# Kernel optimization log

Measured on AMD Instinct MI355X. Metric: run time of the kernel, lower is better.

## Reference

```python
import jax, jax.numpy as jnp
import numpy as np
from functools import partial

STRIDES = (8, 16, 32)
SCORE_THRESH = 0.3
NMS_THRESH = 0.5
TOPK = 500          # fixed pre-NMS candidate count (jit-friendly substitute for boolean masking)
CLASS_OFFSET = 1e4  # offset boxes per class so cross-class IoU == 0 -> per-class NMS


def _decode(cls, reg, obj, stride):
    # cls [B,C,H,W], reg [B,4,H,W], obj [B,1,H,W]
    B, C, H, W = cls.shape
    yv, xv = jnp.meshgrid(jnp.arange(H, dtype=cls.dtype), jnp.arange(W, dtype=cls.dtype), indexing='ij')
    scores = jax.nn.sigmoid(obj) * jax.nn.sigmoid(cls)          # [B,C,H,W]
    dx, dy, dw, dh = reg[:, 0], reg[:, 1], reg[:, 2], reg[:, 3]
    cx = (xv + jax.nn.sigmoid(dx)) * stride
    cy = (yv + jax.nn.sigmoid(dy)) * stride
    w = jnp.exp(dw) * stride
    h = jnp.exp(dh) * stride
    boxes = jnp.stack([cx - w / 2, cy - h / 2, cx + w / 2, cy + h / 2], axis=-1)  # [B,H,W,4]
    return boxes.reshape(B, H * W, 4), scores.reshape(B, C, H * W).transpose(0, 2, 1)


def _pairwise_iou(boxes):
    # boxes [B,K,4] xyxy -> iou [B,K,K]
    area = (boxes[..., 2] - boxes[..., 0]) * (boxes[..., 3] - boxes[..., 1])
    x1 = jnp.maximum(boxes[:, :, None, 0], boxes[:, None, :, 0])
    y1 = jnp.maximum(boxes[:, :, None, 1], boxes[:, None, :, 1])
    x2 = jnp.minimum(boxes[:, :, None, 2], boxes[:, None, :, 2])
    y2 = jnp.minimum(boxes[:, :, None, 3], boxes[:, None, :, 3])
    inter = jnp.clip(x2 - x1, 0) * jnp.clip(y2 - y1, 0)
    union = area[:, :, None] + area[:, None, :] - inter
    return inter / (union + 1e-7)


def _greedy_nms(iou, valid):
    # iou [B,K,K], valid [B,K] -> keep [B,K]; greedy over score-sorted order (axis 1)
    B, K = valid.shape
    def step(supp, i):
        keep_i = valid[:, i] & ~supp[:, i]                    # [B]
        supp = supp | (keep_i[:, None] & (iou[:, i, :] >= NMS_THRESH))
        return supp, keep_i
    _, keep_t = jax.lax.scan(step, jnp.zeros((B, K), dtype=bool), jnp.arange(K))
    return keep_t.T  # [B,K]


def _predict(levels):
    boxes_l, scores_l = [], []
    for (c, r, o), s in zip(levels, STRIDES):
        b, sc = _decode(c, r, o, s)
        boxes_l.append(b)
        scores_l.append(sc)
    boxes = jnp.concatenate(boxes_l, axis=1)     # [B,N,4]
    scores = jnp.concatenate(scores_l, axis=1)   # [B,N,C]
    max_scores = scores.max(axis=-1)             # [B,N]
    labels = jnp.argmax(scores, axis=-1)         # [B,N]
    masked = jnp.where(max_scores > SCORE_THRESH, max_scores, -1.0)
    top_scores, idx = jax.lax.top_k(masked, TOPK)                         # sorted desc
    top_boxes = jnp.take_along_axis(boxes, idx[..., None], axis=1)        # [B,K,4]
    top_labels = jnp.take_along_axis(labels, idx, axis=1)                 # [B,K]
    valid = top_scores > SCORE_THRESH
    boxes_off = top_boxes + (top_labels.astype(top_boxes.dtype) * CLASS_OFFSET)[..., None]
    keep = _greedy_nms(_pairwise_iou(boxes_off), valid)                   # [B,K]
    out_boxes = jnp.where(keep[..., None], top_boxes, 0.0)
    out_scores = jnp.where(keep, top_scores, 0.0)
    return out_boxes, out_scores, top_labels, keep


def setup_inputs() -> dict:
    key = jax.random.key(0)
    ks = jax.random.split(key, 9)
    B, C = 64, 2
    shapes = {
        'cls_p3': (B, C, 160, 160), 'reg_p3': (B, 4, 160, 160), 'obj_p3': (B, 1, 160, 160),
        'cls_p4': (B, C, 80, 80),   'reg_p4': (B, 4, 80, 80),   'obj_p4': (B, 1, 80, 80),
        'cls_p5': (B, C, 40, 40),   'reg_p5': (B, 4, 40, 40),   'obj_p5': (B, 1, 40, 40),
    }
    return {name: jax.random.normal(k, shp, dtype=jnp.float32)
            for k, (name, shp) in zip(ks, shapes.items())}


def reference(cls_p3, reg_p3, obj_p3, cls_p4, reg_p4, obj_p4, cls_p5, reg_p5, obj_p5):
    levels = [(cls_p3, reg_p3, obj_p3), (cls_p4, reg_p4, obj_p4), (cls_p5, reg_p5, obj_p5)]
    return _predict(levels)
```

## Files before the change

### kernel.cpp

```cpp
#include <hip/hip_runtime.h>
#include <hip/hip_bf16.h>
#include <stdint.h>

#define NB 64
#define NA 33600
#define NK 500
#define HW3 25600
#define HW4 6400
#define HW5 1600
#define OFF4 25600
#define OFF5 32000
#define NBIN 2048
#define NA4 8400
#define LCAP 1024
#define MROWS 512

typedef unsigned int u32;
typedef unsigned long long u64;

__device__ __forceinline__ float sigf(float x) { return 1.0f / (1.0f + expf(-x)); }

__device__ __forceinline__ u32 f2key(float f) {
  u32 u = __float_as_uint(f);
  return (u & 0x80000000u) ? ~u : (u | 0x80000000u);
}
__device__ __forceinline__ float key2f(u32 k) {
  u32 u = (k & 0x80000000u) ? (k ^ 0x80000000u) : ~k;
  return __uint_as_float(u);
}
__device__ __forceinline__ int bin_of(float s) {
  int b = (int)(s * 2048.0f);
  return b > 2047 ? 2047 : b;
}
__device__ __forceinline__ u32 mkkey(float o, float c0, float c1) {
  float so = sigf(o);
  float s = fmaxf(so * sigf(c0), so * sigf(c1));
  float masked = (s > 0.3f) ? s : -1.0f;
  return f2key(masked);
}
__device__ __forceinline__ u64 uniform64(u64 v) {
  u32 lo = (u32)__builtin_amdgcn_readfirstlane((int)(u32)v);
  u32 hi = (u32)__builtin_amdgcn_readfirstlane((int)(u32)(v >> 32));
  return ((u64)hi << 32) | lo;
}

__global__ __launch_bounds__(256) void k_score(
    const float* __restrict__ cls3, const float* __restrict__ obj3,
    const float* __restrict__ cls4, const float* __restrict__ obj4,
    const float* __restrict__ cls5, const float* __restrict__ obj5,
    uint4* __restrict__ keys4)
{
  int b = blockIdx.y;
  int i4 = blockIdx.x * 256 + threadIdx.x;
  if (i4 >= NA4) return;
  const float* cls; const float* obj; int p4, HW;
  if (i4 < 6400)      { cls = cls3; obj = obj3; p4 = i4;        HW = HW3; }
  else if (i4 < 8000) { cls = cls4; obj = obj4; p4 = i4 - 6400; HW = HW4; }
  else                { cls = cls5; obj = obj5; p4 = i4 - 8000; HW = HW5; }
  float4 o  = reinterpret_cast<const float4*>(obj + (size_t)b * HW)[p4];
  float4 c0 = reinterpret_cast<const float4*>(cls + (size_t)(b * 2) * HW)[p4];
  float4 c1 = reinterpret_cast<const float4*>(cls + (size_t)(b * 2 + 1) * HW)[p4];
  uint4 kv;
  kv.x = mkkey(o.x, c0.x, c1.x);
  kv.y = mkkey(o.y, c0.y, c1.y);
  kv.z = mkkey(o.z, c0.z, c1.z);
  kv.w = mkkey(o.w, c0.w, c1.w);
  keys4[(size_t)b * NA4 + i4] = kv;
}

__global__ __launch_bounds__(1024) void k_topk(
    const u32* __restrict__ keys,
    const float* __restrict__ cls3, const float* __restrict__ obj3, const float* __restrict__ reg3,
    const float* __restrict__ cls4, const float* __restrict__ obj4, const float* __restrict__ reg4,
    const float* __restrict__ cls5, const float* __restrict__ obj5, const float* __restrict__ reg5,
    float* __restrict__ top_score,
    float4* __restrict__ boxes, float4* __restrict__ boxesoff,
    float* __restrict__ out_labels)
{
  int b = blockIdx.x, tid = threadIdx.x;
  __shared__ u32 hist[NBIN];
  __shared__ u32 part[256];
  __shared__ u64 cand[LCAP];
  __shared__ int idx_lds[NK];
  __shared__ float score_lds[NK];
  __shared__ u32 lcnt;
  __shared__ int sh_p;
  __shared__ u32 sh_R;
  __shared__ int sh_digit;
  __shared__ u32 sh_cnt;

  for (int i = tid; i < NBIN; i += 1024) hist[i] = 0;
  if (tid == 0) lcnt = 0;
  __syncthreads();

  const u32* kb = keys + (size_t)b * NA;
  const uint4* kb4 = reinterpret_cast<const uint4*>(kb);

  uint4 kreg[9];
#pragma unroll
  for (int k = 0; k < 9; ++k) {
    int i4 = tid + k * 1024;
    kreg[k] = (i4 < NA4) ? kb4[i4] : make_uint4(0u, 0u, 0u, 0u);
  }

#pragma unroll
  for (int k = 0; k < 9; ++k) {
    u32 ks[4] = {kreg[k].x, kreg[k].y, kreg[k].z, kreg[k].w};
#pragma unroll
    for (int c = 0; c < 4; ++c) {
      float s = key2f(ks[c]);
      if (s > 0.3f) atomicAdd(&hist[bin_of(s)], 1u);
    }
  }
  __syncthreads();
  if (tid < 256) {
    u32 s8 = 0;
#pragma unroll
    for (int k = 0; k < 8; ++k) s8 += hist[tid * 8 + k];
    part[tid] = s8;
  }
  __syncthreads();
  for (int off = 1; off < 256; off <<= 1) {
    u32 add = 0;
    if (tid < 256 && tid + off < 256) add = part[tid + off];
    __syncthreads();
    if (tid < 256) part[tid] += add;
    __syncthreads();
  }
  if (tid == 0 && part[0] < NK) sh_p = -1;
  if (tid < 256) {
    u32 S = part[tid];
    u32 Snext = (tid == 255) ? 0u : part[tid + 1];
    if (S >= NK && Snext < NK) {
      u32 run = Snext;
      int p = tid * 8;
      for (int k = 7; k >= 0; --k) {
        run += hist[tid * 8 + k];
        if (run >= NK) { p = tid * 8 + k; break; }
      }
      sh_p = p;
    }
  }
  __syncthreads();
  int p = sh_p;
  bool fail = (p < 0);
  if (!fail) {
#pragma unroll
    for (int k = 0; k < 9; ++k) {
      int i4 = tid + k * 1024;
      u32 ks[4] = {kreg[k].x, kreg[k].y, kreg[k].z, kreg[k].w};
#pragma unroll
      for (int c = 0; c < 4; ++c) {
        float s = key2f(ks[c]);
        if (s > 0.3f && bin_of(s) >= p) {
          u32 slot = atomicAdd(&lcnt, 1u);
          if (slot < LCAP) cand[slot] = ((u64)ks[c] << 16) | (u32)(0xFFFF - (i4 * 4 + c));
        }
      }
    }
    __syncthreads();
    fail = (lcnt > LCAP);
  }

  if (!fail) {
    for (int i = lcnt + tid; i < LCAP; i += 1024) cand[i] = 0;
    for (int k = 2; k <= LCAP; k <<= 1) {
      for (int j = k >> 1; j > 0; j >>= 1) {
        __syncthreads();
        if (tid < LCAP / 2) {
          int i = ((tid & ~(j - 1)) << 1) | (tid & (j - 1));
          int ixj = i | j;
          u64 a = cand[i], c2 = cand[ixj];
          bool dir = ((i & k) == 0);
          if ((a < c2) == dir) { cand[i] = c2; cand[ixj] = a; }
        }
      }
    }
    __syncthreads();
    if (tid < NK) {
      u64 kk = cand[tid];
      idx_lds[tid] = 0xFFFF - (int)(kk & 0xFFFFull);
      score_lds[tid] = key2f((u32)(kk >> 16));
    }
  } else {
    u64 prefix = 0, prefmask = 0;
    u32 R = NK;
    for (int pass = 0; pass < 6; ++pass) {
      int shift = 40 - 8 * pass;
      if (tid < 256) part[tid] = 0;
      __syncthreads();
      for (int i = tid; i < NA; i += 1024) {
        u64 k48 = ((u64)kb[i] << 16) | (u32)(0xFFFF - i);
        if ((k48 & prefmask) == prefix)
          atomicAdd(&part[(u32)(k48 >> shift) & 255u], 1u);
      }
      __syncthreads();
      if (tid < 256) hist[tid] = part[tid];
      __syncthreads();
      for (int off = 1; off < 256; off <<= 1) {
        u32 add = 0;
        if (tid < 256 && tid + off < 256) add = hist[tid + off];
        __syncthreads();
        if (tid < 256) hist[tid] += add;
        __syncthreads();
      }
      if (tid < 256) {
        u32 s = hist[tid];
        u32 snext = (tid == 255) ? 0u : hist[tid + 1];
        if (s >= R && snext < R) { sh_digit = tid; sh_R = R - snext; }
      }
      __syncthreads();
      prefix |= ((u64)sh_digit) << shift;
      R = sh_R;
      prefmask |= 0xFFull << shift;
      __syncthreads();
    }
    if (tid == 0) sh_cnt = 0;
    if (tid < NK) { idx_lds[tid] = 0; score_lds[tid] = -1.0f; }
    __syncthreads();
    for (int i = tid; i < NA; i += 1024) {
      u64 k48 = ((u64)kb[i] << 16) | (u32)(0xFFFF - i);
      if (k48 >= prefix) {
        u32 slot = atomicAdd(&sh_cnt, 1u);
        if (slot < 512) cand[slot] = k48;
      }
    }
    __syncthreads();
    int n = (sh_cnt < (u32)NK) ? (int)sh_cnt : NK;
    for (int t = tid; t < n; t += 1024) {
      u64 k = cand[t];
      int rank = 0;
      for (int j = 0; j < n; ++j) rank += (cand[j] > k) ? 1 : 0;
      if (rank < NK) {
        idx_lds[rank] = 0xFFFF - (int)(k & 0xFFFFull);
        score_lds[rank] = key2f((u32)(k >> 16));
      }
    }
  }
  __syncthreads();

  if (tid < NK) {
    int a = idx_lds[tid];
    const float *cls, *obj, *reg; int pos, HW, x, y; float stride;
    if (a < OFF4) {
      cls = cls3; obj = obj3; reg = reg3; pos = a; HW = HW3; stride = 8.0f;
      y = pos / 160; x = pos - y * 160;
    } else if (a < OFF5) {
      cls = cls4; obj = obj4; reg = reg4; pos = a - OFF4; HW = HW4; stride = 16.0f;
      y = pos / 80; x = pos - y * 80;
    } else {
      cls = cls5; obj = obj5; reg = reg5; pos = a - OFF5; HW = HW5; stride = 32.0f;
      y = pos / 40; x = pos - y * 40;
    }
    float dx = reg[(b * 4 + 0) * HW + pos];
    float dy = reg[(b * 4 + 1) * HW + pos];
    float dw = reg[(b * 4 + 2) * HW + pos];
    float dh = reg[(b * 4 + 3) * HW + pos];
    float cx = ((float)x + sigf(dx)) * stride;
    float cy = ((float)y + sigf(dy)) * stride;
    float w = expf(dw) * stride;
    float h = expf(dh) * stride;
    float x1 = cx - w * 0.5f, y1 = cy - h * 0.5f;
    float x2 = cx + w * 0.5f, y2 = cy + h * 0.5f;
    float so = sigf(obj[b * HW + pos]);
    float s0 = so * sigf(cls[(b * 2) * HW + pos]);
    float s1 = so * sigf(cls[(b * 2 + 1) * HW + pos]);
    int label = (s1 > s0) ? 1 : 0;
    float off = (float)label * 10000.0f;
    int t = b * NK + tid;
    boxes[t]    = make_float4(x1, y1, x2, y2);
    boxesoff[t] = make_float4(x1 + off, y1 + off, x2 + off, y2 + off);
    out_labels[t] = (float)label;
    top_score[t] = score_lds[tid];
  }
}

__global__ __launch_bounds__(256) void k_iou(
    const float4* __restrict__ boxesoff, u64* __restrict__ mask)
{
  int t = blockIdx.x * 256 + threadIdx.x;
  if (t >= NB * NK * 8) return;
  int w = t & 7;
  int bi = t >> 3;
  int b = bi / NK;
  int i = bi - b * NK;
  float4 A = boxesoff[bi];
  float areaA = (A.z - A.x) * (A.w - A.y);
  const float4* base = boxesoff + b * NK;
  int j0 = w * 64;
  int jmax = (NK - j0 < 64) ? (NK - j0) : 64;
  u64 bits = 0;
  for (int jj = 0; jj < jmax; ++jj) {
    float4 Bx = base[j0 + jj];
    float areaB = (Bx.z - Bx.x) * (Bx.w - Bx.y);
    float ix1 = fmaxf(A.x, Bx.x);
    float iy1 = fmaxf(A.y, Bx.y);
    float ix2 = fminf(A.z, Bx.z);
    float iy2 = fminf(A.w, Bx.w);
    float iw = fmaxf(ix2 - ix1, 0.0f);
    float ih = fmaxf(iy2 - iy1, 0.0f);
    float inter = iw * ih;
    float uni = areaA + areaB - inter;
    float iou = inter / (uni + 1e-7f);
    bits |= ((u64)(iou >= 0.5f)) << jj;
  }
  mask[(size_t)b * (MROWS * 8) + (size_t)i * 8 + w] = bits;
}

__global__ __launch_bounds__(64) void k_nms(
    const u64* __restrict__ mask, const float* __restrict__ top_score,
    const float4* __restrict__ boxes,
    float* __restrict__ out_boxes, float* __restrict__ out_scores,
    float* __restrict__ out_keep)
{
  int b = blockIdx.x;
  int lane = threadIdx.x;
  const u64* mb = mask + (size_t)b * (MROWS * 8);

  u64 validw[8];
#pragma unroll
  for (int c = 0; c < 8; ++c) {
    int r = c * 64 + lane;
    float s = (r < NK) ? top_score[b * NK + r] : -1.0f;
    validw[c] = __ballot(s > 0.3f);
  }

  u64 supp[8] = {0, 0, 0, 0, 0, 0, 0, 0};
  u64 keepw[8];
  u64 row[2][8];

  {
    const u64* rp = mb + (size_t)lane * 8;
#pragma unroll
    for (int w = 0; w < 8; ++w) row[0][w] = rp[w];
  }

#pragma unroll
  for (int c = 0; c < 8; ++c) {
    const int cur = c & 1, nxt = cur ^ 1;
    if (c < 7) {
      const u64* rp = mb + (size_t)((c + 1) * 64 + lane) * 8;
#pragma unroll
      for (int w = 0; w < 8; ++w)
        if (w >= c + 1) row[nxt][w] = rp[w];
    }
    u32 rlo = (u32)row[cur][c];
    u32 rhi = (u32)(row[cur][c] >> 32);
    u64 sw = supp[c], vw = validw[c], km = 0;
#pragma unroll
    for (int i = 0; i < 64; ++i) {
      u64 wi = ((u64)(u32)__builtin_amdgcn_readlane(rhi, i) << 32) |
               (u64)(u32)__builtin_amdgcn_readlane(rlo, i);
      u64 bit = 1ull << i;
      if ((vw & bit) && !(sw & bit)) { sw |= wi; km |= bit; }
    }
    keepw[c] = km;
    u64 sel = ((km >> lane) & 1ull) ? ~0ull : 0ull;
#pragma unroll
    for (int w = c + 1; w < 8; ++w) {
      u64 v = row[cur][w] & sel;
#pragma unroll
      for (int off = 1; off < 64; off <<= 1)
        v |= (u64)__shfl_xor((unsigned long long)v, off, 64);
      supp[w] |= uniform64(v);
    }
  }

#pragma unroll
  for (int c = 0; c < 8; ++c) {
    int r = c * 64 + lane;
    if (r < NK) {
      int kp = (int)((keepw[c] >> lane) & 1ull);
      float4 bx = boxes[b * NK + r];
      float s = top_score[b * NK + r];
      float4 ob;
      ob.x = kp ? bx.x : 0.0f;
      ob.y = kp ? bx.y : 0.0f;
      ob.z = kp ? bx.z : 0.0f;
      ob.w = kp ? bx.w : 0.0f;
      reinterpret_cast<float4*>(out_boxes)[b * NK + r] = ob;
      out_scores[b * NK + r] = kp ? s : 0.0f;
      out_keep[b * NK + r]   = kp ? 1.0f : 0.0f;
    }
  }
}

extern "C" void kernel_launch(void* const* d_in, const int* in_sizes, int n_in,
                              void* d_out, int out_size, void* d_ws, size_t ws_size,
                              hipStream_t stream) {
  const float* cls3 = (const float*)d_in[0];
  const float* reg3 = (const float*)d_in[1];
  const float* obj3 = (const float*)d_in[2];
  const float* cls4 = (const float*)d_in[3];
  const float* reg4 = (const float*)d_in[4];
  const float* obj4 = (const float*)d_in[5];
  const float* cls5 = (const float*)d_in[6];
  const float* reg5 = (const float*)d_in[7];
  const float* obj5 = (const float*)d_in[8];

  char* ws = (char*)d_ws;
  u32*    keys      = (u32*)   (ws + 0);
  float*  top_score = (float*) (ws + 8601600);
  float4* boxes     = (float4*)(ws + 8729600);
  float4* boxesoff  = (float4*)(ws + 9241600);
  u64*    mask      = (u64*)   (ws + 9753600);

  float* out        = (float*)d_out;
  float* out_boxes  = out;
  float* out_scores = out + 128000;
  float* out_labels = out + 160000;
  float* out_keep   = out + 192000;

  dim3 gscore((NA4 + 255) / 256, NB);
  k_score<<<gscore, 256, 0, stream>>>(cls3, obj3, cls4, obj4, cls5, obj5, (uint4*)keys);
  k_topk<<<NB, 1024, 0, stream>>>(keys,
      cls3, obj3, reg3, cls4, obj4, reg4, cls5, obj5, reg5,
      top_score, boxes, boxesoff, out_labels);
  k_iou<<<(NB * NK * 8 + 255) / 256, 256, 0, stream>>>(boxesoff, mask);
  k_nms<<<NB, 64, 0, stream>>>(mask, top_score, boxes, out_boxes, out_scores, out_keep);
}
```

Measured before the change: 95.10 us.

## Fuse score/key computation into top-k kernel and reuse keys from registers

```diff
diff --git a/kernel.cpp b/kernel.cpp
--- a/kernel.cpp
+++ b/kernel.cpp
@@ -44,32 +44,7 @@
   return ((u64)hi << 32) | lo;
 }
 
-__global__ __launch_bounds__(256) void k_score(
-    const float* __restrict__ cls3, const float* __restrict__ obj3,
-    const float* __restrict__ cls4, const float* __restrict__ obj4,
-    const float* __restrict__ cls5, const float* __restrict__ obj5,
-    uint4* __restrict__ keys4)
-{
-  int b = blockIdx.y;
-  int i4 = blockIdx.x * 256 + threadIdx.x;
-  if (i4 >= NA4) return;
-  const float* cls; const float* obj; int p4, HW;
-  if (i4 < 6400)      { cls = cls3; obj = obj3; p4 = i4;        HW = HW3; }
-  else if (i4 < 8000) { cls = cls4; obj = obj4; p4 = i4 - 6400; HW = HW4; }
-  else                { cls = cls5; obj = obj5; p4 = i4 - 8000; HW = HW5; }
-  float4 o  = reinterpret_cast<const float4*>(obj + (size_t)b * HW)[p4];
-  float4 c0 = reinterpret_cast<const float4*>(cls + (size_t)(b * 2) * HW)[p4];
-  float4 c1 = reinterpret_cast<const float4*>(cls + (size_t)(b * 2 + 1) * HW)[p4];
-  uint4 kv;
-  kv.x = mkkey(o.x, c0.x, c1.x);
-  kv.y = mkkey(o.y, c0.y, c1.y);
-  kv.z = mkkey(o.z, c0.z, c1.z);
-  kv.w = mkkey(o.w, c0.w, c1.w);
-  keys4[(size_t)b * NA4 + i4] = kv;
-}
-
 __global__ __launch_bounds__(1024) void k_topk(
-    const u32* __restrict__ keys,
     const float* __restrict__ cls3, const float* __restrict__ obj3, const float* __restrict__ reg3,
     const float* __restrict__ cls4, const float* __restrict__ obj4, const float* __restrict__ reg4,
     const float* __restrict__ cls5, const float* __restrict__ obj5, const float* __restrict__ reg5,
@@ -93,14 +68,25 @@
   if (tid == 0) lcnt = 0;
   __syncthreads();
 
-  const u32* kb = keys + (size_t)b * NA;
-  const uint4* kb4 = reinterpret_cast<const uint4*>(kb);
-
   uint4 kreg[9];
 #pragma unroll
   for (int k = 0; k < 9; ++k) {
     int i4 = tid + k * 1024;
-    kreg[k] = (i4 < NA4) ? kb4[i4] : make_uint4(0u, 0u, 0u, 0u);
+    uint4 kv = make_uint4(0u, 0u, 0u, 0u);
+    if (i4 < NA4) {
+      const float* cls; const float* obj; int p4, HW;
+      if (i4 < 6400)      { cls = cls3; obj = obj3; p4 = i4;        HW = HW3; }
+      else if (i4 < 8000) { cls = cls4; obj = obj4; p4 = i4 - 6400; HW = HW4; }
+      else                { cls = cls5; obj = obj5; p4 = i4 - 8000; HW = HW5; }
+      float4 o  = reinterpret_cast<const float4*>(obj + (size_t)b * HW)[p4];
+      float4 c0 = reinterpret_cast<const float4*>(cls + (size_t)(b * 2) * HW)[p4];
+      float4 c1 = reinterpret_cast<const float4*>(cls + (size_t)(b * 2 + 1) * HW)[p4];
+      kv.x = mkkey(o.x, c0.x, c1.x);
+      kv.y = mkkey(o.y, c0.y, c1.y);
+      kv.z = mkkey(o.z, c0.z, c1.z);
+      kv.w = mkkey(o.w, c0.w, c1.w);
+    }
+    kreg[k] = kv;
   }
 
 #pragma unroll
@@ -189,10 +175,18 @@
       int shift = 40 - 8 * pass;
       if (tid < 256) part[tid] = 0;
       __syncthreads();
-      for (int i = tid; i < NA; i += 1024) {
-        u64 k48 = ((u64)kb[i] << 16) | (u32)(0xFFFF - i);
-        if ((k48 & prefmask) == prefix)
-          atomicAdd(&part[(u32)(k48 >> shift) & 255u], 1u);
+#pragma unroll
+      for (int k = 0; k < 9; ++k) {
+        int i4 = tid + k * 1024;
+        if (i4 < NA4) {
+          u32 ks[4] = {kreg[k].x, kreg[k].y, kreg[k].z, kreg[k].w};
+#pragma unroll
+          for (int c = 0; c < 4; ++c) {
+            u64 k48 = ((u64)ks[c] << 16) | (u32)(0xFFFF - (i4 * 4 + c));
+            if ((k48 & prefmask) == prefix)
+              atomicAdd(&part[(u32)(k48 >> shift) & 255u], 1u);
+          }
+        }
       }
       __syncthreads();
       if (tid < 256) hist[tid] = part[tid];
@@ -218,11 +212,19 @@
     if (tid == 0) sh_cnt = 0;
     if (tid < NK) { idx_lds[tid] = 0; score_lds[tid] = -1.0f; }
     __syncthreads();
-    for (int i = tid; i < NA; i += 1024) {
-      u64 k48 = ((u64)kb[i] << 16) | (u32)(0xFFFF - i);
-      if (k48 >= prefix) {
-        u32 slot = atomicAdd(&sh_cnt, 1u);
-        if (slot < 512) cand[slot] = k48;
+#pragma unroll
+    for (int k = 0; k < 9; ++k) {
+      int i4 = tid + k * 1024;
+      if (i4 < NA4) {
+        u32 ks[4] = {kreg[k].x, kreg[k].y, kreg[k].z, kreg[k].w};
+#pragma unroll
+        for (int c = 0; c < 4; ++c) {
+          u64 k48 = ((u64)ks[c] << 16) | (u32)(0xFFFF - (i4 * 4 + c));
+          if (k48 >= prefix) {
+            u32 slot = atomicAdd(&sh_cnt, 1u);
+            if (slot < 512) cand[slot] = k48;
+          }
+        }
       }
     }
     __syncthreads();
@@ -347,7 +349,7 @@
     u32 rlo = (u32)row[cur][c];
     u32 rhi = (u32)(row[cur][c] >> 32);
     u64 sw = supp[c], vw = validw[c], km = 0;
-#pragma unroll
+#pragma unroll 1
     for (int i = 0; i < 64; ++i) {
       u64 wi = ((u64)(u32)__builtin_amdgcn_readlane(rhi, i) << 32) |
                (u64)(u32)__builtin_amdgcn_readlane(rlo, i);
@@ -399,11 +401,10 @@
   const float* obj5 = (const float*)d_in[8];
 
   char* ws = (char*)d_ws;
-  u32*    keys      = (u32*)   (ws + 0);
-  float*  top_score = (float*) (ws + 8601600);
-  float4* boxes     = (float4*)(ws + 8729600);
-  float4* boxesoff  = (float4*)(ws + 9241600);
-  u64*    mask      = (u64*)   (ws + 9753600);
+  float*  top_score = (float*) (ws + 0);
+  float4* boxes     = (float4*)(ws + 128000);
+  float4* boxesoff  = (float4*)(ws + 640000);
+  u64*    mask      = (u64*)   (ws + 1152000);
 
   float* out        = (float*)d_out;
   float* out_boxes  = out;
@@ -411,9 +412,7 @@
   float* out_labels = out + 160000;
   float* out_keep   = out + 192000;
 
-  dim3 gscore((NA4 + 255) / 256, NB);
-  k_score<<<gscore, 256, 0, stream>>>(cls3, obj3, cls4, obj4, cls5, obj5, (uint4*)keys);
-  k_topk<<<NB, 1024, 0, stream>>>(keys,
+  k_topk<<<NB, 1024, 0, stream>>>(
       cls3, obj3, reg3, cls4, obj4, reg4, cls5, obj5, reg5,
       top_score, boxes, boxesoff, out_labels);
   k_iou<<<(NB * NK * 8 + 255) / 256, 256, 0, stream>>>(boxesoff, mask);
```

New measurement: 117.3 us. +23.3%, slower.

## Split top-k into grid-wide histogram, pivot, and collect kernels; defer NMS OR-reductions

Applied to the files above, without the earlier changes.

```diff
diff --git a/kernel.cpp b/kernel.cpp
--- a/kernel.cpp
+++ b/kernel.cpp
@@ -10,11 +10,13 @@
 #define HW5 1600
 #define OFF4 25600
 #define OFF5 32000
-#define NBIN 2048
 #define NA4 8400
+#define NSEG 33
+#define NBIN 256
 #define LCAP 1024
 #define MROWS 512
 
+typedef unsigned short u16;
 typedef unsigned int u32;
 typedef unsigned long long u64;
 
@@ -29,8 +31,8 @@
   return __uint_as_float(u);
 }
 __device__ __forceinline__ int bin_of(float s) {
-  int b = (int)(s * 2048.0f);
-  return b > 2047 ? 2047 : b;
+  int b = (int)(s * 256.0f);
+  return b > 255 ? 255 : b;
 }
 __device__ __forceinline__ u32 mkkey(float o, float c0, float c1) {
   float so = sigf(o);
@@ -48,28 +50,110 @@
     const float* __restrict__ cls3, const float* __restrict__ obj3,
     const float* __restrict__ cls4, const float* __restrict__ obj4,
     const float* __restrict__ cls5, const float* __restrict__ obj5,
-    uint4* __restrict__ keys4)
-{
-  int b = blockIdx.y;
-  int i4 = blockIdx.x * 256 + threadIdx.x;
-  if (i4 >= NA4) return;
-  const float* cls; const float* obj; int p4, HW;
-  if (i4 < 6400)      { cls = cls3; obj = obj3; p4 = i4;        HW = HW3; }
-  else if (i4 < 8000) { cls = cls4; obj = obj4; p4 = i4 - 6400; HW = HW4; }
-  else                { cls = cls5; obj = obj5; p4 = i4 - 8000; HW = HW5; }
-  float4 o  = reinterpret_cast<const float4*>(obj + (size_t)b * HW)[p4];
-  float4 c0 = reinterpret_cast<const float4*>(cls + (size_t)(b * 2) * HW)[p4];
-  float4 c1 = reinterpret_cast<const float4*>(cls + (size_t)(b * 2 + 1) * HW)[p4];
-  uint4 kv;
-  kv.x = mkkey(o.x, c0.x, c1.x);
-  kv.y = mkkey(o.y, c0.y, c1.y);
-  kv.z = mkkey(o.z, c0.z, c1.z);
-  kv.w = mkkey(o.w, c0.w, c1.w);
-  keys4[(size_t)b * NA4 + i4] = kv;
-}
-
-__global__ __launch_bounds__(1024) void k_topk(
-    const u32* __restrict__ keys,
+    uint4* __restrict__ keys4, u16* __restrict__ ghist_part)
+{
+  int seg = blockIdx.x, b = blockIdx.y, tid = threadIdx.x;
+  int i4 = seg * 256 + tid;
+  __shared__ u32 hist[NBIN];
+  hist[tid] = 0;
+  __syncthreads();
+
+  if (i4 < NA4) {
+    const float* cls; const float* obj; int p4, HW;
+    if (i4 < 6400)      { cls = cls3; obj = obj3; p4 = i4;        HW = HW3; }
+    else if (i4 < 8000) { cls = cls4; obj = obj4; p4 = i4 - 6400; HW = HW4; }
+    else                { cls = cls5; obj = obj5; p4 = i4 - 8000; HW = HW5; }
+    float4 o  = reinterpret_cast<const float4*>(obj + (size_t)b * HW)[p4];
+    float4 c0 = reinterpret_cast<const float4*>(cls + (size_t)(b * 2) * HW)[p4];
+    float4 c1 = reinterpret_cast<const float4*>(cls + (size_t)(b * 2 + 1) * HW)[p4];
+    uint4 kv;
+    kv.x = mkkey(o.x, c0.x, c1.x);
+    kv.y = mkkey(o.y, c0.y, c1.y);
+    kv.z = mkkey(o.z, c0.z, c1.z);
+    kv.w = mkkey(o.w, c0.w, c1.w);
+    keys4[(size_t)b * NA4 + i4] = kv;
+    u32 ks[4] = {kv.x, kv.y, kv.z, kv.w};
+#pragma unroll
+    for (int c = 0; c < 4; ++c) {
+      float s = key2f(ks[c]);
+      if (s > 0.3f) atomicAdd(&hist[bin_of(s)], 1u);
+    }
+  }
+  __syncthreads();
+  if (tid < 128) {
+    u32 pk = (hist[2 * tid] & 0xFFFFu) | (hist[2 * tid + 1] << 16);
+    reinterpret_cast<u32*>(ghist_part + ((size_t)(b * NSEG + seg) * NBIN))[tid] = pk;
+  }
+}
+
+__global__ __launch_bounds__(256) void k_pivot(
+    const u16* __restrict__ ghist_part,
+    int* __restrict__ pivot, int* __restrict__ ok, u32* __restrict__ cnt)
+{
+  int b = blockIdx.x, t = threadIdx.x;
+  __shared__ u32 part[NBIN];
+  __shared__ int sh_p, sh_ok;
+  u32 sum = 0;
+  for (int seg = 0; seg < NSEG; ++seg)
+    sum += ghist_part[(size_t)(b * NSEG + seg) * NBIN + t];
+  part[t] = sum;
+  __syncthreads();
+  for (int off = 1; off < NBIN; off <<= 1) {
+    u32 add = (t + off < NBIN) ? part[t + off] : 0u;
+    __syncthreads();
+    part[t] += add;
+    __syncthreads();
+  }
+  if (t == 0 && part[0] < NK) { sh_p = -1; sh_ok = 0; }
+  u32 S = part[t];
+  u32 Snext = (t == NBIN - 1) ? 0u : part[t + 1];
+  if (S >= NK && Snext < NK) {
+    sh_p = t;
+    sh_ok = (S <= LCAP) ? 1 : 0;
+  }
+  __syncthreads();
+  if (t == 0) { pivot[b] = sh_p; ok[b] = sh_ok; cnt[b] = 0; }
+}
+
+__global__ __launch_bounds__(256) void k_collect(
+    const u32* __restrict__ keys, const int* __restrict__ pivot, const int* __restrict__ ok,
+    u64* __restrict__ cand, u32* __restrict__ cnt)
+{
+  int seg = blockIdx.x, b = blockIdx.y, tid = threadIdx.x;
+  if (!ok[b]) return;
+  int p = pivot[b];
+  __shared__ u64 loc[1024];
+  __shared__ u32 lcnt;
+  __shared__ u32 gbase;
+  if (tid == 0) lcnt = 0;
+  __syncthreads();
+
+  int i4 = seg * 256 + tid;
+  if (i4 < NA4) {
+    uint4 kv = reinterpret_cast<const uint4*>(keys + (size_t)b * NA)[i4];
+    u32 ks[4] = {kv.x, kv.y, kv.z, kv.w};
+#pragma unroll
+    for (int c = 0; c < 4; ++c) {
+      float s = key2f(ks[c]);
+      if (s > 0.3f && bin_of(s) >= p) {
+        u32 slot = atomicAdd(&lcnt, 1u);
+        loc[slot] = ((u64)ks[c] << 16) | (u32)(0xFFFF - (i4 * 4 + c));
+      }
+    }
+  }
+  __syncthreads();
+  if (tid == 0) gbase = atomicAdd(&cnt[b], lcnt);
+  __syncthreads();
+  u32 n = lcnt, gb = gbase;
+  for (u32 i = tid; i < n; i += 256) {
+    u32 slot = gb + i;
+    if (slot < LCAP) cand[(size_t)b * LCAP + slot] = loc[i];
+  }
+}
+
+__global__ __launch_bounds__(1024) void k_sortdec(
+    const u32* __restrict__ keys, const u64* __restrict__ gcand,
+    const u32* __restrict__ cnt, const int* __restrict__ ok,
     const float* __restrict__ cls3, const float* __restrict__ obj3, const float* __restrict__ reg3,
     const float* __restrict__ cls4, const float* __restrict__ obj4, const float* __restrict__ reg4,
     const float* __restrict__ cls5, const float* __restrict__ obj5, const float* __restrict__ reg5,
@@ -78,92 +162,22 @@
     float* __restrict__ out_labels)
 {
   int b = blockIdx.x, tid = threadIdx.x;
-  __shared__ u32 hist[NBIN];
-  __shared__ u32 part[256];
   __shared__ u64 cand[LCAP];
   __shared__ int idx_lds[NK];
   __shared__ float score_lds[NK];
-  __shared__ u32 lcnt;
-  __shared__ int sh_p;
+  __shared__ u32 hist[256];
+  __shared__ u32 part[256];
   __shared__ u32 sh_R;
   __shared__ int sh_digit;
   __shared__ u32 sh_cnt;
 
-  for (int i = tid; i < NBIN; i += 1024) hist[i] = 0;
-  if (tid == 0) lcnt = 0;
-  __syncthreads();
-
+  u32 n = cnt[b];
+  bool fail = (!ok[b]) || (n > LCAP);
   const u32* kb = keys + (size_t)b * NA;
-  const uint4* kb4 = reinterpret_cast<const uint4*>(kb);
-
-  uint4 kreg[9];
-#pragma unroll
-  for (int k = 0; k < 9; ++k) {
-    int i4 = tid + k * 1024;
-    kreg[k] = (i4 < NA4) ? kb4[i4] : make_uint4(0u, 0u, 0u, 0u);
-  }
-
-#pragma unroll
-  for (int k = 0; k < 9; ++k) {
-    u32 ks[4] = {kreg[k].x, kreg[k].y, kreg[k].z, kreg[k].w};
-#pragma unroll
-    for (int c = 0; c < 4; ++c) {
-      float s = key2f(ks[c]);
-      if (s > 0.3f) atomicAdd(&hist[bin_of(s)], 1u);
-    }
-  }
-  __syncthreads();
-  if (tid < 256) {
-    u32 s8 = 0;
-#pragma unroll
-    for (int k = 0; k < 8; ++k) s8 += hist[tid * 8 + k];
-    part[tid] = s8;
-  }
-  __syncthreads();
-  for (int off = 1; off < 256; off <<= 1) {
-    u32 add = 0;
-    if (tid < 256 && tid + off < 256) add = part[tid + off];
-    __syncthreads();
-    if (tid < 256) part[tid] += add;
-    __syncthreads();
-  }
-  if (tid == 0 && part[0] < NK) sh_p = -1;
-  if (tid < 256) {
-    u32 S = part[tid];
-    u32 Snext = (tid == 255) ? 0u : part[tid + 1];
-    if (S >= NK && Snext < NK) {
-      u32 run = Snext;
-      int p = tid * 8;
-      for (int k = 7; k >= 0; --k) {
-        run += hist[tid * 8 + k];
-        if (run >= NK) { p = tid * 8 + k; break; }
-      }
-      sh_p = p;
-    }
-  }
-  __syncthreads();
-  int p = sh_p;
-  bool fail = (p < 0);
+
   if (!fail) {
-#pragma unroll
-    for (int k = 0; k < 9; ++k) {
-      int i4 = tid + k * 1024;
-      u32 ks[4] = {kreg[k].x, kreg[k].y, kreg[k].z, kreg[k].w};
-#pragma unroll
-      for (int c = 0; c < 4; ++c) {
-        float s = key2f(ks[c]);
-        if (s > 0.3f && bin_of(s) >= p) {
-          u32 slot = atomicAdd(&lcnt, 1u);
-          if (slot < LCAP) cand[slot] = ((u64)ks[c] << 16) | (u32)(0xFFFF - (i4 * 4 + c));
-        }
-      }
-    }
-    __syncthreads();
-    fail = (lcnt > LCAP);
-  }
-
-  if (!fail) {
-    for (int i = lcnt + tid; i < LCAP; i += 1024) cand[i] = 0;
+    for (int i = tid; i < LCAP; i += 1024)
+      cand[i] = (i < (int)n) ? gcand[(size_t)b * LCAP + i] : 0ull;
     for (int k = 2; k <= LCAP; k <<= 1) {
       for (int j = k >> 1; j > 0; j >>= 1) {
         __syncthreads();
@@ -226,11 +240,11 @@
       }
     }
     __syncthreads();
-    int n = (sh_cnt < (u32)NK) ? (int)sh_cnt : NK;
-    for (int t = tid; t < n; t += 1024) {
+    int m = (sh_cnt < (u32)NK) ? (int)sh_cnt : NK;
+    for (int t = tid; t < m; t += 1024) {
       u64 k = cand[t];
       int rank = 0;
-      for (int j = 0; j < n; ++j) rank += (cand[j] > k) ? 1 : 0;
+      for (int j = 0; j < m; ++j) rank += (cand[j] > k) ? 1 : 0;
       if (rank < NK) {
         idx_lds[rank] = 0xFFFF - (int)(k & 0xFFFFull);
         score_lds[rank] = key2f((u32)(k >> 16));
@@ -325,7 +339,7 @@
     validw[c] = __ballot(s > 0.3f);
   }
 
-  u64 supp[8] = {0, 0, 0, 0, 0, 0, 0, 0};
+  u64 Sw[8] = {0, 0, 0, 0, 0, 0, 0, 0};
   u64 keepw[8];
   u64 row[2][8];
 
@@ -344,10 +358,16 @@
       for (int w = 0; w < 8; ++w)
         if (w >= c + 1) row[nxt][w] = rp[w];
     }
+    u64 v = Sw[c];
+#pragma unroll
+    for (int off = 1; off < 64; off <<= 1)
+      v |= (u64)__shfl_xor((unsigned long long)v, off, 64);
+    u64 sw = uniform64(v);
+
     u32 rlo = (u32)row[cur][c];
     u32 rhi = (u32)(row[cur][c] >> 32);
-    u64 sw = supp[c], vw = validw[c], km = 0;
-#pragma unroll
+    u64 vw = validw[c], km = 0;
+#pragma unroll 1
     for (int i = 0; i < 64; ++i) {
       u64 wi = ((u64)(u32)__builtin_amdgcn_readlane(rhi, i) << 32) |
                (u64)(u32)__builtin_amdgcn_readlane(rlo, i);
@@ -357,13 +377,8 @@
     keepw[c] = km;
     u64 sel = ((km >> lane) & 1ull) ? ~0ull : 0ull;
 #pragma unroll
-    for (int w = c + 1; w < 8; ++w) {
-      u64 v = row[cur][w] & sel;
-#pragma unroll
-      for (int off = 1; off < 64; off <<= 1)
-        v |= (u64)__shfl_xor((unsigned long long)v, off, 64);
-      supp[w] |= uniform64(v);
-    }
+    for (int w = c + 1; w < 8; ++w)
+      Sw[w] |= row[cur][w] & sel;
   }
 
 #pragma unroll
@@ -400,10 +415,15 @@
 
   char* ws = (char*)d_ws;
   u32*    keys      = (u32*)   (ws + 0);
-  float*  top_score = (float*) (ws + 8601600);
-  float4* boxes     = (float4*)(ws + 8729600);
-  float4* boxesoff  = (float4*)(ws + 9241600);
-  u64*    mask      = (u64*)   (ws + 9753600);
+  u16*    ghist     = (u16*)   (ws + 8601600);
+  int*    pivot     = (int*)   (ws + 9682944);
+  int*    ok        = (int*)   (ws + 9683200);
+  u32*    cnt       = (u32*)   (ws + 9683456);
+  u64*    cand      = (u64*)   (ws + 9683712);
+  float*  top_score = (float*) (ws + 10208000);
+  float4* boxes     = (float4*)(ws + 10336000);
+  float4* boxesoff  = (float4*)(ws + 10848000);
+  u64*    mask      = (u64*)   (ws + 11360000);
 
   float* out        = (float*)d_out;
   float* out_boxes  = out;
@@ -411,9 +431,12 @@
   float* out_labels = out + 160000;
   float* out_keep   = out + 192000;
 
-  dim3 gscore((NA4 + 255) / 256, NB);
-  k_score<<<gscore, 256, 0, stream>>>(cls3, obj3, cls4, obj4, cls5, obj5, (uint4*)keys);
-  k_topk<<<NB, 1024, 0, stream>>>(keys,
+  dim3 gfull(NSEG, NB);
+  k_score<<<gfull, 256, 0, stream>>>(cls3, obj3, cls4, obj4, cls5, obj5,
+                                     (uint4*)keys, ghist);
+  k_pivot<<<NB, 256, 0, stream>>>(ghist, pivot, ok, cnt);
+  k_collect<<<gfull, 256, 0, stream>>>(keys, pivot, ok, cand, cnt);
+  k_sortdec<<<NB, 1024, 0, stream>>>(keys, cand, cnt, ok,
       cls3, obj3, reg3, cls4, obj4, reg4, cls5, obj5, reg5,
       top_score, boxes, boxesoff, out_labels);
   k_iou<<<(NB * NK * 8 + 255) / 256, 256, 0, stream>>>(boxesoff, mask);
```

After: 117.0 us. 1.23x slower.
